# Performance work log

Measured on AMD Instinct MI355X. Metric: run time of the kernel, lower is better.

## Reference

```python
import jax, jax.numpy as jnp
import numpy as np

N, S, T, E, H = 4, 2048, 2048, 512, 8
HD = E // H  # head_dim = 64


def setup_inputs() -> dict:
    key0 = jax.random.key(0)
    ks = jax.random.split(key0, 12)
    sc = 1.0 / np.sqrt(E)
    inp = {
        "query": jax.random.normal(ks[0], (N, S, E), jnp.float32),
        "key": jax.random.normal(ks[1], (N, T, E), jnp.float32),
        "value": jax.random.normal(ks[2], (N, T, E), jnp.float32),
        "attn_mask": jnp.tril(jnp.ones((S, T), jnp.int32)),  # causal: 0 => masked
        # nn.Linear weights (out, in) and biases, torch convention y = x @ W.T + b
        "Wq": jax.random.normal(ks[3], (E, E), jnp.float32) * sc,
        "bq": jax.random.normal(ks[4], (E,), jnp.float32) * sc,
        "Wk": jax.random.normal(ks[5], (E, E), jnp.float32) * sc,
        "bk": jax.random.normal(ks[6], (E,), jnp.float32) * sc,
        "Wv": jax.random.normal(ks[7], (E, E), jnp.float32) * sc,
        "bv": jax.random.normal(ks[8], (E,), jnp.float32) * sc,
        "Wp": jax.random.normal(ks[9], (E, E), jnp.float32) * sc,
        "bp": jax.random.normal(ks[10], (E,), jnp.float32) * sc,
    }
    return inp


def reference(query, key, value, attn_mask, Wq, bq, Wk, bk, Wv, bv, Wp, bp):
    # QKV projections, split heads: (N, H, L, HD)
    q = (query @ Wq.T + bq).reshape(N, S, H, HD).transpose(0, 2, 1, 3)
    k = (key @ Wk.T + bk).reshape(N, T, H, HD).transpose(0, 2, 1, 3)
    v = (value @ Wv.T + bv).reshape(N, T, H, HD).transpose(0, 2, 1, 3)
    # scaled scores (N, H, S, T) -- intentionally materialized like the original
    e = jnp.einsum("nhsd,nhtd->nhst", q, k) / jnp.sqrt(jnp.float32(HD))
    e = jnp.where(attn_mask == 0, -jnp.inf, e)
    a = jax.nn.softmax(e, axis=-1)
    # dropout is identity in eval mode (reference runs deterministic/eval)
    y = jnp.einsum("nhst,nhtd->nhsd", a, v)
    y = y.transpose(0, 2, 1, 3).reshape(N, S, E)
    return y @ Wp.T + bp
```

## Files before the change

kernel.cpp:

```cpp
#include <hip/hip_runtime.h>


#define DEV __device__ __forceinline__

typedef unsigned short u16;
typedef unsigned int u32;
typedef __bf16 bf16x8 __attribute__((ext_vector_type(8)));
typedef float f32x4 __attribute__((ext_vector_type(4)));
typedef float f32x16 __attribute__((ext_vector_type(16)));

#define MFMA16(A, B, C) __builtin_amdgcn_mfma_f32_16x16x32_bf16(A, B, C, 0, 0, 0)
#define MFMA32(A, B, C) __builtin_amdgcn_mfma_f32_32x32x16_bf16(A, B, C, 0, 0, 0)

#define SC 0.18033688f

DEV u16 f2bf(float f) {
  u32 u = __builtin_bit_cast(u32, f);
  u += 0x7fffu + ((u >> 16) & 1u);
  return (u16)(u >> 16);
}
DEV u16 f2bf_ru(float f) {
  u32 u = __builtin_bit_cast(u32, f);
  return (u16)((u + 0x8000u) >> 16);
}

DEV void cp16(void* l, const void* g) {
  __builtin_amdgcn_global_load_lds(
      (const __attribute__((address_space(1))) u32*)g,
      (__attribute__((address_space(3))) u32*)l, 16, 0, 0);
}

__global__ __launch_bounds__(256) void cast_all(
    const float* __restrict__ q, const float* __restrict__ k, const float* __restrict__ v,
    const float* __restrict__ wq, const float* __restrict__ wk, const float* __restrict__ wv,
    const float* __restrict__ wp,
    u16* qo, u16* ko, u16* vo, u16* wqo, u16* wko, u16* wvo, u16* wpo) {
  int b = blockIdx.x, tid = threadIdx.x;
  const float* s;
  u16* d;
  int off;
  float sc = 1.f;
  if (b < 12288) {
    int which = b >> 12;
    s = (which == 0) ? q : (which == 1) ? k : v;
    d = (which == 0) ? qo : (which == 1) ? ko : vo;
    off = (b & 4095) * 256;
  } else {
    int wb = b - 12288, which = wb >> 8;
    s = (which == 0) ? wq : (which == 1) ? wk : (which == 2) ? wv : wp;
    d = (which == 0) ? wqo : (which == 1) ? wko : (which == 2) ? wvo : wpo;
    off = (wb & 255) * 256;
    if (which == 0) sc = SC;
  }
  int i = off + tid;
  float4 f = ((const float4*)s)[i];
  ushort4 o;
  o.x = f2bf(f.x * sc); o.y = f2bf(f.y * sc); o.z = f2bf(f.z * sc); o.w = f2bf(f.w * sc);
  ((ushort4*)d)[i] = o;
}

DEV void gemm_loop(const u16* __restrict__ A, const u16* __restrict__ W,
                   u16* As, u16* Bs, int m0, int n0, int tid, f32x4 acc[4][4]) {
  const int lane = tid & 63, wid = tid >> 6;
  const int wm = wid & 1, wn = wid >> 1;
  const int l15 = lane & 15, l4 = lane >> 4;
  for (int kt = 0; kt < 512; kt += 32) {
    __syncthreads();
#pragma unroll
    for (int i = 0; i < 2; ++i) {
      int c = tid + 256 * i;
      int row = c >> 2, kc = (c & 3) * 8;
      cp16(&As[c * 8], A + (m0 + row) * 512 + kt + kc);
      cp16(&Bs[c * 8], W + (n0 + row) * 512 + kt + kc);
    }
    __syncthreads();
    bf16x8 af[4], bfr[4];
#pragma unroll
    for (int f = 0; f < 4; ++f) {
      af[f]  = *(const bf16x8*)&As[(wm * 64 + f * 16 + l15) * 32 + l4 * 8];
      bfr[f] = *(const bf16x8*)&Bs[(wn * 64 + f * 16 + l15) * 32 + l4 * 8];
    }
#pragma unroll
    for (int fm = 0; fm < 4; ++fm)
#pragma unroll
      for (int fn = 0; fn < 4; ++fn)
        acc[fm][fn] = MFMA16(af[fm], bfr[fn], acc[fm][fn]);
  }
}

__global__ __launch_bounds__(256) void gemm_qkv(
    const u16* __restrict__ qx, const u16* __restrict__ kx, const u16* __restrict__ vx,
    const u16* __restrict__ wq, const u16* __restrict__ wk, const u16* __restrict__ wv,
    const float* __restrict__ bq, const float* __restrict__ bk, const float* __restrict__ bv,
    u16* qp, u16* kp, u16* vt) {
  __shared__ u16 As[128 * 32];
  __shared__ u16 Bs[128 * 32];
  const int wsel = blockIdx.x >> 2;
  const u16* A = (wsel == 0) ? qx : (wsel == 1) ? kx : vx;
  const u16* W = (wsel == 0) ? wq : (wsel == 1) ? wk : wv;
  const float* bias = (wsel == 0) ? bq : (wsel == 1) ? bk : bv;
  const int n0 = (blockIdx.x & 3) * 128, m0 = blockIdx.y * 128;
  const int tid = threadIdx.x, lane = tid & 63, wid = tid >> 6;
  const int wm = wid & 1, wn = wid >> 1;
  const int l15 = lane & 15, l4 = lane >> 4;

  f32x4 acc[4][4] = {};
  gemm_loop(A, W, As, Bs, m0, n0, tid, acc);

  if (wsel < 2) {
    u16* C = (wsel == 0) ? qp : kp;
    const float bscale = (wsel == 0) ? SC : 1.f;
#pragma unroll
    for (int fn = 0; fn < 4; ++fn) {
      int col = n0 + wn * 64 + fn * 16 + l15;
      float bvv = bias[col] * bscale;
#pragma unroll
      for (int fm = 0; fm < 4; ++fm) {
        int rowb = m0 + wm * 64 + fm * 16 + l4 * 4;
#pragma unroll
        for (int r = 0; r < 4; ++r)
          C[(rowb + r) * 512 + col] = f2bf(acc[fm][fn][r] + bvv);
      }
    }
  } else {
    const int nIdx = m0 >> 11, tb = m0 & 2047;
#pragma unroll
    for (int fn = 0; fn < 4; ++fn) {
      int col = n0 + wn * 64 + fn * 16 + l15;
      int vtrow = (nIdx * 8 + (col >> 6)) * 64 + (col & 63);
      float bvv = bias[col];
#pragma unroll
      for (int fm = 0; fm < 4; ++fm) {
        int t = tb + wm * 64 + fm * 16 + l4 * 4;
        ushort4 o;
        o.x = f2bf(acc[fm][fn][0] + bvv);
        o.y = f2bf(acc[fm][fn][1] + bvv);
        o.z = f2bf(acc[fm][fn][2] + bvv);
        o.w = f2bf(acc[fm][fn][3] + bvv);
        *(ushort4*)(vt + vtrow * 2048 + t) = o;
      }
    }
  }
}

__global__ __launch_bounds__(256) void gemm_out(const u16* __restrict__ A,
                                                const u16* __restrict__ W,
                                                const float* __restrict__ bias,
                                                float* __restrict__ C) {
  __shared__ u16 As[128 * 32];
  __shared__ u16 Bs[128 * 32];
  const int n0 = blockIdx.x * 128, m0 = blockIdx.y * 128;
  const int tid = threadIdx.x, lane = tid & 63, wid = tid >> 6;
  const int wm = wid & 1, wn = wid >> 1;
  const int l15 = lane & 15, l4 = lane >> 4;

  f32x4 acc[4][4] = {};
  gemm_loop(A, W, As, Bs, m0, n0, tid, acc);

#pragma unroll
  for (int fn = 0; fn < 4; ++fn) {
    int col = n0 + wn * 64 + fn * 16 + l15;
    float bvv = bias[col];
#pragma unroll
    for (int fm = 0; fm < 4; ++fm) {
      int rowb = m0 + wm * 64 + fm * 16 + l4 * 4;
#pragma unroll
      for (int r = 0; r < 4; ++r)
        C[(rowb + r) * 512 + col] = acc[fm][fn][r] + bvv;
    }
  }
}

__global__ __launch_bounds__(256) void attn_kernel(const u16* __restrict__ Qg,
                                                   const u16* __restrict__ Kg,
                                                   const u16* __restrict__ Vt,
                                                   u16* __restrict__ Yg) {
  __shared__ u16 Ps[128 * 128];
  __shared__ u16 Ks[128 * 64];
  __shared__ u16 Vs[64 * 128];

  const int bid = blockIdx.x;
  const int nh = bid & 31;
  const int p = bid >> 5;
  const int qt = (p < 8) ? (15 - p) : (p - 8);
  const int n = nh >> 3, h = nh & 7;
  const int tid = threadIdx.x, lane = tid & 63, w = tid >> 6;
  const int l31 = lane & 31, lh = lane >> 5;
  const int s0 = qt * 128;

  const u16* Qb = Qg + (n * 2048 + s0) * 512 + h * 64;
  const u16* Kb = Kg + n * 2048 * 512 + h * 64;
  const u16* Vb = Vt + nh * 64 * 2048;

#pragma unroll
  for (int i = 0; i < 4; ++i) {
    int ci = tid + 256 * i;
    int m = ci >> 3, pc = ci & 7;
    cp16(&Ps[ci * 8], Qb + m * 512 + ((pc ^ (m & 7)) * 8));
  }
  __syncthreads();
  const int qm = w * 32 + l31;
  bf16x8 qf[4];
#pragma unroll
  for (int ks = 0; ks < 4; ++ks)
    qf[ks] = *(const bf16x8*)&Ps[qm * 64 + (((2 * ks + lh) ^ (qm & 7)) * 8)];

  f32x16 accO[2] = {};
  float mrow = -1e30f, lrow = 0.f;

  for (int it = 0; it <= qt; ++it) {
    const int t0 = it * 128;
    __syncthreads();
#pragma unroll
    for (int i = 0; i < 4; ++i) {
      int ci = tid + 256 * i;
      int t = ci >> 3, pc = ci & 7;
      cp16(&Ks[ci * 8], Kb + (t0 + t) * 512 + ((pc ^ (t & 7)) * 8));
    }
#pragma unroll
    for (int i = 0; i < 4; ++i) {
      int ci = tid + 256 * i;
      int d = ci >> 4, pc = ci & 15;
      cp16(&Vs[ci * 8], Vb + d * 2048 + t0 + ((pc ^ (d & 15)) * 8));
    }
    __syncthreads();

    const bool diag = (it == qt);
    const int nf = diag ? (w + 1) : 4;

    f32x16 st[4];
#pragma unroll
    for (int f = 0; f < 4; ++f)
      if (f < nf) {
        f32x16 a = {};
        int tr = f * 32 + l31;
#pragma unroll
        for (int ks = 0; ks < 4; ++ks) {
          bf16x8 kf = *(const bf16x8*)&Ks[tr * 64 + (((2 * ks + lh) ^ (tr & 7)) * 8)];
          a = MFMA32(kf, qf[ks], a);
        }
        if (diag && f == w) {
#pragma unroll
          for (int r = 0; r < 16; ++r) {
            int trow = f * 32 + (r & 3) + 8 * (r >> 2) + 4 * lh;
            a[r] = (trow > qm) ? -1e30f : a[r];
          }
        }
        st[f] = a;
      }

    float rmax = -1e30f;
#pragma unroll
    for (int f = 0; f < 4; ++f)
      if (f < nf)
#pragma unroll
        for (int r = 0; r < 16; ++r) rmax = fmaxf(rmax, st[f][r]);
    rmax = fmaxf(rmax, __shfl_xor(rmax, 32));
    float mnew = fmaxf(mrow, rmax);
    float alpha = __builtin_amdgcn_exp2f(mrow - mnew);
    mrow = mnew;
    float rsum = 0.f;
#pragma unroll
    for (int f = 0; f < 4; ++f)
      if (f < nf)
#pragma unroll
        for (int r = 0; r < 16; ++r) {
          float pv = __builtin_amdgcn_exp2f(st[f][r] - mnew);
          st[f][r] = pv;
          rsum += pv;
        }
    rsum += __shfl_xor(rsum, 32);
    lrow = lrow * alpha + rsum;
    accO[0] = accO[0] * alpha;
    accO[1] = accO[1] * alpha;

    const int pbase = qm * 128;
#pragma unroll
    for (int f = 0; f < 4; ++f)
      if (f < nf)
#pragma unroll
        for (int g = 0; g < 4; ++g) {
          ushort4 pk;
          pk.x = f2bf_ru(st[f][4 * g + 0]);
          pk.y = f2bf_ru(st[f][4 * g + 1]);
          pk.z = f2bf_ru(st[f][4 * g + 2]);
          pk.w = f2bf_ru(st[f][4 * g + 3]);
          int c8 = f * 8 + 2 * g + lh;
          *(ushort4*)&Ps[pbase + ((c8 ^ (qm & 31)) * 4)] = pk;
        }

    const int nks = nf * 2;
#pragma unroll
    for (int ks = 0; ks < 8; ++ks)
      if (ks < nks) {
        int c8a = 4 * ks + 2 * lh;
        uint2 lo = *(const uint2*)&Ps[pbase + ((c8a ^ (qm & 31)) * 4)];
        uint2 hi = *(const uint2*)&Ps[pbase + (((c8a + 1) ^ (qm & 31)) * 4)];
        uint4 pb4;
        pb4.x = lo.x; pb4.y = lo.y; pb4.z = hi.x; pb4.w = hi.y;
        bf16x8 pb = __builtin_bit_cast(bf16x8, pb4);
#pragma unroll
        for (int fd = 0; fd < 2; ++fd) {
          int d = fd * 32 + l31;
          bf16x8 vf = *(const bf16x8*)&Vs[d * 128 + (((2 * ks + lh) ^ (d & 15)) * 8)];
          accO[fd] = MFMA32(vf, pb, accO[fd]);
        }
      }
  }

  float inv = 1.0f / lrow;
  u16* Yb = Yg + (n * 2048 + s0 + qm) * 512 + h * 64;
#pragma unroll
  for (int fd = 0; fd < 2; ++fd)
#pragma unroll
    for (int g = 0; g < 4; ++g) {
      ushort4 o;
      o.x = f2bf(accO[fd][4 * g + 0] * inv);
      o.y = f2bf(accO[fd][4 * g + 1] * inv);
      o.z = f2bf(accO[fd][4 * g + 2] * inv);
      o.w = f2bf(accO[fd][4 * g + 3] * inv);
      *(ushort4*)(Yb + fd * 32 + 8 * g + 4 * lh) = o;
    }
}

extern "C" void kernel_launch(void* const* d_in, const int* in_sizes, int n_in,
                              void* d_out, int out_size, void* d_ws, size_t ws_size,
                              hipStream_t stream) {
  (void)in_sizes; (void)n_in; (void)out_size; (void)ws_size;
  const float* query = (const float*)d_in[0];
  const float* key_  = (const float*)d_in[1];
  const float* value = (const float*)d_in[2];
  const float* Wq = (const float*)d_in[4];
  const float* bq = (const float*)d_in[5];
  const float* Wk = (const float*)d_in[6];
  const float* bk = (const float*)d_in[7];
  const float* Wv = (const float*)d_in[8];
  const float* bv = (const float*)d_in[9];
  const float* Wp = (const float*)d_in[10];
  const float* bp = (const float*)d_in[11];

  char* ws = (char*)d_ws;
  u16* qx  = (u16*)(ws);
  u16* kx  = (u16*)(ws + 8388608);
  u16* vx  = (u16*)(ws + 16777216);
  u16* wqx = (u16*)(ws + 25165824);
  u16* wkx = (u16*)(ws + 25690112);
  u16* wvx = (u16*)(ws + 26214400);
  u16* wpx = (u16*)(ws + 26738688);
  u16* qp  = (u16*)(ws + 27262976);
  u16* kp  = (u16*)(ws + 35651584);
  u16* vt  = (u16*)(ws + 44040192);
  u16* y   = qx;

  cast_all<<<13312, 256, 0, stream>>>(query, key_, value, Wq, Wk, Wv, Wp,
                                      qx, kx, vx, wqx, wkx, wvx, wpx);
  gemm_qkv<<<dim3(12, 64), 256, 0, stream>>>(qx, kx, vx, wqx, wkx, wvx,
                                             bq, bk, bv, qp, kp, vt);
  attn_kernel<<<512, 256, 0, stream>>>(qp, kp, vt, y);
  gemm_out<<<dim3(4, 64), 256, 0, stream>>>(y, wpx, bp, (float*)d_out);
}
```

Measured before the change: 225.6 us.

## Keep softmax P in registers via lane shuffles; transpose V projection GEMM

```diff
diff --git a/kernel.cpp b/kernel.cpp
--- a/kernel.cpp
+++ b/kernel.cpp
@@ -19,9 +19,10 @@
   u += 0x7fffu + ((u >> 16) & 1u);
   return (u16)(u >> 16);
 }
-DEV u16 f2bf_ru(float f) {
-  u32 u = __builtin_bit_cast(u32, f);
-  return (u16)((u + 0x8000u) >> 16);
+DEV u32 pk2(float lo, float hi) {
+  u32 a = __builtin_bit_cast(u32, lo) + 0x8000u;
+  u32 b = __builtin_bit_cast(u32, hi) + 0x8000u;
+  return __builtin_amdgcn_perm(b, a, 0x07060302u);
 }
 
 DEV void cp16(void* l, const void* g) {
@@ -96,10 +97,12 @@
   __shared__ u16 As[128 * 32];
   __shared__ u16 Bs[128 * 32];
   const int wsel = blockIdx.x >> 2;
-  const u16* A = (wsel == 0) ? qx : (wsel == 1) ? kx : vx;
-  const u16* W = (wsel == 0) ? wq : (wsel == 1) ? wk : wv;
+  const int xq = blockIdx.x & 3;
+  const u16* A = (wsel == 0) ? qx : (wsel == 1) ? kx : wv;
+  const u16* W = (wsel == 0) ? wq : (wsel == 1) ? wk : vx;
   const float* bias = (wsel == 0) ? bq : (wsel == 1) ? bk : bv;
-  const int n0 = (blockIdx.x & 3) * 128, m0 = blockIdx.y * 128;
+  const int m0 = (wsel == 2) ? xq * 128 : blockIdx.y * 128;
+  const int n0 = (wsel == 2) ? blockIdx.y * 128 : xq * 128;
   const int tid = threadIdx.x, lane = tid & 63, wid = tid >> 6;
   const int wm = wid & 1, wn = wid >> 1;
   const int l15 = lane & 15, l4 = lane >> 4;
@@ -123,21 +126,21 @@
       }
     }
   } else {
-    const int nIdx = m0 >> 11, tb = m0 & 2047;
-#pragma unroll
-    for (int fn = 0; fn < 4; ++fn) {
-      int col = n0 + wn * 64 + fn * 16 + l15;
-      int vtrow = (nIdx * 8 + (col >> 6)) * 64 + (col & 63);
-      float bvv = bias[col];
-#pragma unroll
-      for (int fm = 0; fm < 4; ++fm) {
-        int t = tb + wm * 64 + fm * 16 + l4 * 4;
-        ushort4 o;
-        o.x = f2bf(acc[fm][fn][0] + bvv);
-        o.y = f2bf(acc[fm][fn][1] + bvv);
-        o.z = f2bf(acc[fm][fn][2] + bvv);
-        o.w = f2bf(acc[fm][fn][3] + bvv);
-        *(ushort4*)(vt + vtrow * 2048 + t) = o;
+    const int nIdx = n0 >> 11;
+    const int tb = n0 & 2047;
+#pragma unroll
+    for (int fm = 0; fm < 4; ++fm) {
+      int rowb = m0 + wm * 64 + fm * 16 + l4 * 4;
+#pragma unroll
+      for (int r = 0; r < 4; ++r) {
+        int row = rowb + r;
+        float bvv = bias[row];
+        int vtrow = (nIdx * 8 + (row >> 6)) * 64 + (row & 63);
+#pragma unroll
+        for (int fn = 0; fn < 4; ++fn) {
+          int tcol = tb + wn * 64 + fn * 16 + l15;
+          vt[vtrow * 2048 + tcol] = f2bf(acc[fm][fn][r] + bvv);
+        }
       }
     }
   }
@@ -175,7 +178,6 @@
                                                    const u16* __restrict__ Kg,
                                                    const u16* __restrict__ Vt,
                                                    u16* __restrict__ Yg) {
-  __shared__ u16 Ps[128 * 128];
   __shared__ u16 Ks[128 * 64];
   __shared__ u16 Vs[64 * 128];
 
@@ -196,14 +198,14 @@
   for (int i = 0; i < 4; ++i) {
     int ci = tid + 256 * i;
     int m = ci >> 3, pc = ci & 7;
-    cp16(&Ps[ci * 8], Qb + m * 512 + ((pc ^ (m & 7)) * 8));
+    cp16(&Ks[ci * 8], Qb + m * 512 + ((pc ^ (m & 7)) * 8));
   }
   __syncthreads();
   const int qm = w * 32 + l31;
   bf16x8 qf[4];
 #pragma unroll
   for (int ks = 0; ks < 4; ++ks)
-    qf[ks] = *(const bf16x8*)&Ps[qm * 64 + (((2 * ks + lh) ^ (qm & 7)) * 8)];
+    qf[ks] = *(const bf16x8*)&Ks[qm * 64 + (((2 * ks + lh) ^ (qm & 7)) * 8)];
 
   f32x16 accO[2] = {};
   float mrow = -1e30f, lrow = 0.f;
@@ -259,51 +261,51 @@
     float mnew = fmaxf(mrow, rmax);
     float alpha = __builtin_amdgcn_exp2f(mrow - mnew);
     mrow = mnew;
+    accO[0] = accO[0] * alpha;
+    accO[1] = accO[1] * alpha;
+
     float rsum = 0.f;
+    u32 pd[4][8];
 #pragma unroll
     for (int f = 0; f < 4; ++f)
-      if (f < nf)
+      if (f < nf) {
 #pragma unroll
         for (int r = 0; r < 16; ++r) {
           float pv = __builtin_amdgcn_exp2f(st[f][r] - mnew);
           st[f][r] = pv;
           rsum += pv;
         }
+#pragma unroll
+        for (int g = 0; g < 4; ++g) {
+          pd[f][2 * g]     = pk2(st[f][4 * g + 0], st[f][4 * g + 1]);
+          pd[f][2 * g + 1] = pk2(st[f][4 * g + 2], st[f][4 * g + 3]);
+        }
+      }
     rsum += __shfl_xor(rsum, 32);
     lrow = lrow * alpha + rsum;
-    accO[0] = accO[0] * alpha;
-    accO[1] = accO[1] * alpha;
-
-    const int pbase = qm * 128;
+
 #pragma unroll
     for (int f = 0; f < 4; ++f)
-      if (f < nf)
-#pragma unroll
-        for (int g = 0; g < 4; ++g) {
-          ushort4 pk;
-          pk.x = f2bf_ru(st[f][4 * g + 0]);
-          pk.y = f2bf_ru(st[f][4 * g + 1]);
-          pk.z = f2bf_ru(st[f][4 * g + 2]);
-          pk.w = f2bf_ru(st[f][4 * g + 3]);
-          int c8 = f * 8 + 2 * g + lh;
-          *(ushort4*)&Ps[pbase + ((c8 ^ (qm & 31)) * 4)] = pk;
-        }
-
-    const int nks = nf * 2;
-#pragma unroll
-    for (int ks = 0; ks < 8; ++ks)
-      if (ks < nks) {
-        int c8a = 4 * ks + 2 * lh;
-        uint2 lo = *(const uint2*)&Ps[pbase + ((c8a ^ (qm & 31)) * 4)];
-        uint2 hi = *(const uint2*)&Ps[pbase + (((c8a + 1) ^ (qm & 31)) * 4)];
-        uint4 pb4;
-        pb4.x = lo.x; pb4.y = lo.y; pb4.z = hi.x; pb4.w = hi.y;
-        bf16x8 pb = __builtin_bit_cast(bf16x8, pb4);
-#pragma unroll
-        for (int fd = 0; fd < 2; ++fd) {
-          int d = fd * 32 + l31;
-          bf16x8 vf = *(const bf16x8*)&Vs[d * 128 + (((2 * ks + lh) ^ (d & 15)) * 8)];
-          accO[fd] = MFMA32(vf, pb, accO[fd]);
+      if (f < nf) {
+#pragma unroll
+        for (int hh = 0; hh < 2; ++hh) {
+          u32 s0 = lh ? pd[f][4 * hh + 0] : pd[f][4 * hh + 2];
+          u32 s1 = lh ? pd[f][4 * hh + 1] : pd[f][4 * hh + 3];
+          u32 r0 = __shfl_xor(s0, 32);
+          u32 r1 = __shfl_xor(s1, 32);
+          uint4 b4;
+          b4.x = lh ? r0 : pd[f][4 * hh + 0];
+          b4.y = lh ? r1 : pd[f][4 * hh + 1];
+          b4.z = lh ? pd[f][4 * hh + 2] : r0;
+          b4.w = lh ? pd[f][4 * hh + 3] : r1;
+          bf16x8 pb = __builtin_bit_cast(bf16x8, b4);
+          const int ks = 2 * f + hh;
+#pragma unroll
+          for (int fd = 0; fd < 2; ++fd) {
+            int d = fd * 32 + l31;
+            bf16x8 vf = *(const bf16x8*)&Vs[d * 128 + (((2 * ks + lh) ^ (d & 15)) * 8)];
+            accO[fd] = MFMA32(vf, pb, accO[fd]);
+          }
         }
       }
   }
```

After: 221.9 us. About the same (-1.6%).
